# Performance work log

Hardware: AMD Instinct MI355X
Metric: run time of the kernel (lower is better)

Reference implementation:

```python
import jax, jax.numpy as jnp
import numpy as np

HEAD_DIM = 64
N_HEADS = 16
D_S = N_HEADS * HEAD_DIM  # 1024
D_Z = 128


def setup_inputs() -> dict:
    key = jax.random.key(0)
    ks = jax.random.split(key, 12)
    B, S = 1, 1024
    sc = 0.02
    return {
        "s": jax.random.normal(ks[0], (B, S, D_S), jnp.float32),
        "z": jax.random.normal(ks[1], (B, S, S, D_Z), jnp.float32),
        "wq": jax.random.normal(ks[2], (N_HEADS * HEAD_DIM, D_S), jnp.float32) * sc,
        "bq": jax.random.normal(ks[3], (N_HEADS * HEAD_DIM,), jnp.float32) * sc,
        "wk": jax.random.normal(ks[4], (N_HEADS * HEAD_DIM, D_S), jnp.float32) * sc,
        "wv": jax.random.normal(ks[5], (N_HEADS * HEAD_DIM, D_S), jnp.float32) * sc,
        "wg": jax.random.normal(ks[6], (N_HEADS * HEAD_DIM, D_S), jnp.float32) * sc,
        "z_norm_w": jnp.ones((D_Z,), jnp.float32),
        "z_norm_b": jnp.zeros((D_Z,), jnp.float32),
        "wz": jax.random.normal(ks[7], (N_HEADS, D_Z), jnp.float32) * sc,
        "wo": jax.random.normal(ks[8], (D_S, N_HEADS * HEAD_DIM), jnp.float32) * sc,
    }


def _layer_norm(x, w, b, eps=1e-5):
    mu = jnp.mean(x, axis=-1, keepdims=True)
    var = jnp.var(x, axis=-1, keepdims=True)
    return (x - mu) * jax.lax.rsqrt(var + eps) * w + b


def reference(s, z, wq, bq, wk, wv, wg, z_norm_w, z_norm_b, wz, wo):
    B, S, _ = s.shape
    H, hd = N_HEADS, HEAD_DIM
    # fused QKV projection (only q has bias in the original)
    q = (s @ wq.T + bq).reshape(B, S, H, hd)
    k = (s @ wk.T).reshape(B, S, H, hd)
    v = (s @ wv.T).reshape(B, S, H, hd)
    # pair bias: LN(z) -> linear D_Z -> H, permute to [B,H,S,S]
    zn = _layer_norm(z, z_norm_w, z_norm_b)
    bias = jnp.einsum("bijz,hz->bhij", zn, wz)  # [B,H,S,S]
    # attention with pair bias (net math: qk/sqrt(d) + bias)
    scores = jnp.einsum("bihd,bjhd->bhij", q, k) * (hd ** -0.5) + bias
    attn = jax.nn.softmax(scores, axis=-1)
    o = jnp.einsum("bhij,bjhd->bihd", attn, v).reshape(B, S, H * hd)
    # sigmoid gate then output projection
    g = jax.nn.sigmoid(s @ wg.T)
    return (o * g) @ wo.T
```

## Files before the change

### kernel.cpp

```cpp
#include <hip/hip_runtime.h>

typedef __attribute__((ext_vector_type(8))) short bf16x8;
typedef __attribute__((ext_vector_type(4))) float f32x4;

#define MFMA16(a,b,c) __builtin_amdgcn_mfma_f32_16x16x32_bf16(a,b,c,0,0,0)

__device__ __forceinline__ unsigned short f2bf(float f){
  unsigned int u = __float_as_uint(f);
  unsigned int r = (u + 0x7fffu + ((u >> 16) & 1u)) >> 16;
  return (unsigned short)r;
}
__device__ __forceinline__ float bf2f(unsigned short u){
  return __uint_as_float(((unsigned int)u) << 16);
}

__global__ __launch_bounds__(256) void prep_kernel(
    const float* __restrict__ s, const float* __restrict__ wq,
    const float* __restrict__ wk, const float* __restrict__ wv,
    const float* __restrict__ wg, const float* __restrict__ wo,
    unsigned short* __restrict__ sb, unsigned short* __restrict__ Wp,
    unsigned short* __restrict__ wob)
{
  const size_t M1 = 1u << 20;
  size_t base = ((size_t)blockIdx.x * 256 + threadIdx.x) * 4;
  const float* src; unsigned short* dst; size_t off;
  if (base < M1) { src = s; dst = sb; off = base; }
  else if (base < 5*M1) {
    size_t r = base - M1; int wsel = (int)(r >> 20);
    const float* wsrc0 = (wsel == 0) ? wq : (wsel == 1) ? wk : (wsel == 2) ? wv : wg;
    src = wsrc0; dst = Wp + ((size_t)wsel << 20); off = r & (M1 - 1);
  } else { src = wo; dst = wob; off = base - 5*M1; }
  float4 v = *(const float4*)(src + off);
  ushort4 o4;
  o4.x = f2bf(v.x); o4.y = f2bf(v.y); o4.z = f2bf(v.z); o4.w = f2bf(v.w);
  *(ushort4*)(dst + off) = o4;
}

__global__ __launch_bounds__(256) void wzprep_kernel(
    const float* __restrict__ wz, const float* __restrict__ znw,
    const float* __restrict__ znb, unsigned short* __restrict__ wzp,
    float* __restrict__ c12)
{
  __shared__ float r1[256], r2[256];
  int t = threadIdx.x; int h = t >> 4; int k0 = (t & 15) * 8;
  float p1 = 0.f, p2 = 0.f;
  for (int e = 0; e < 8; e++) {
    float wv = wz[h*128 + k0 + e];
    float w = znw[k0 + e], b = znb[k0 + e];
    wzp[h*128 + k0 + e] = f2bf(wv * w);
    p1 += wv * w; p2 += wv * b;
  }
  r1[t] = p1; r2[t] = p2;
  __syncthreads();
  if ((t & 15) == 0) {
    float s1 = 0.f, s2 = 0.f;
    for (int i = 0; i < 16; i++) { s1 += r1[t + i]; s2 += r2[t + i]; }
    c12[2*h] = s1; c12[2*h + 1] = s2;
  }
}

template<int MODE>
__global__ __launch_bounds__(256) void gemm_bf16(
    const unsigned short* __restrict__ A, const unsigned short* __restrict__ Bm,
    int M, int N, int K,
    const float* __restrict__ bq,
    unsigned short* __restrict__ qb, unsigned short* __restrict__ kb,
    unsigned short* __restrict__ vT, unsigned short* __restrict__ gb,
    float* __restrict__ outF)
{
  int lane = threadIdx.x & 63;
  int w = threadIdx.x >> 6;
  int lr = lane & 15, lg = lane >> 4;
  int row0 = blockIdx.y * 64 + (w & 1) * 32;
  int col0 = blockIdx.x * 128 + (w >> 1) * 64;
  f32x4 acc[2][4] = {};
  for (int kk = 0; kk < K; kk += 32) {
    bf16x8 af[2], bfr[4];
    #pragma unroll
    for (int t = 0; t < 2; t++)
      af[t] = *(const bf16x8*)(A + (size_t)(row0 + t*16 + lr) * K + kk + lg*8);
    #pragma unroll
    for (int t = 0; t < 4; t++)
      bfr[t] = *(const bf16x8*)(Bm + (size_t)(col0 + t*16 + lr) * K + kk + lg*8);
    #pragma unroll
    for (int a = 0; a < 2; a++)
      #pragma unroll
      for (int b = 0; b < 4; b++)
        acc[a][b] = MFMA16(af[a], bfr[b], acc[a][b]);
  }
  #pragma unroll
  for (int a = 0; a < 2; a++)
    #pragma unroll
    for (int b = 0; b < 4; b++)
      #pragma unroll
      for (int r = 0; r < 4; r++) {
        int m = row0 + a*16 + lg*4 + r;
        int n = col0 + b*16 + lr;
        float v = acc[a][b][r];
        if (MODE == 0) {
          if (n < 1024)      { v = (v + bq[n]) * 0.125f; qb[(size_t)m*1024 + n] = f2bf(v); }
          else if (n < 2048) { kb[(size_t)m*1024 + (n-1024)] = f2bf(v); }
          else if (n < 3072) { vT[(size_t)(n-2048)*1024 + m] = f2bf(v); }
          else               { float sg = 1.f / (1.f + __expf(-v)); gb[(size_t)m*1024 + (n-3072)] = f2bf(sg); }
        } else {
          outF[(size_t)m * N + n] = v;
        }
      }
}

__global__ __launch_bounds__(1024, 4) void fused_attn(
    const unsigned short* __restrict__ qb, const unsigned short* __restrict__ kb,
    const unsigned short* __restrict__ vT, const float* __restrict__ z,
    const unsigned short* __restrict__ wzp, const float* __restrict__ c12,
    float* __restrict__ op, float* __restrict__ ml, float* __restrict__ ll)
{
  __shared__ float biasT[16][16][68];
  __shared__ unsigned short P[16][1024];
  int w = threadIdx.x >> 6;
  int lane = threadIdx.x & 63;
  int jl = lane & 15, g = lane >> 4;
  int q0 = blockIdx.x * 16;
  int s = blockIdx.y;
  int h = w;
  unsigned short* Pw = P[w];

  bf16x8 af[4];
  #pragma unroll
  for (int mk = 0; mk < 4; mk++)
    af[mk] = *(const bf16x8*)(wzp + jl*128 + mk*32 + g*8);
  bf16x8 aq[2];
  #pragma unroll
  for (int kh = 0; kh < 2; kh++)
    aq[kh] = *(const bf16x8*)(qb + (size_t)(q0 + jl)*1024 + h*64 + kh*32 + g*8);
  float c1r[4], c2r[4];
  #pragma unroll
  for (int r = 0; r < 4; r++) {
    c1r[r] = c12[2*(g*4 + r)];
    c2r[r] = c12[2*(g*4 + r) + 1];
  }

  f32x4 od[4] = {};
  float m = -1e30f, ss = 0.f;

  for (int t = 0; t < 4; t++) {
    int jt = s*256 + t*64;

    #pragma unroll
    for (int it = 0; it < 4; it++) {
      int j = jt + it*16 + jl;
      const float* zp = z + ((size_t)(q0 + w)*1024 + j)*128;
      float4 zv[8];
      #pragma unroll
      for (int mk = 0; mk < 4; mk++) {
        zv[2*mk]   = *(const float4*)(zp + mk*32 + g*8);
        zv[2*mk+1] = *(const float4*)(zp + mk*32 + g*8 + 4);
      }
      float sum = 0.f, sq = 0.f;
      #pragma unroll
      for (int u = 0; u < 8; u++) {
        float4 v = zv[u];
        sum += v.x + v.y + v.z + v.w;
        sq = fmaf(v.x, v.x, fmaf(v.y, v.y, fmaf(v.z, v.z, fmaf(v.w, v.w, sq))));
      }
      sum += __shfl_xor(sum, 16); sum += __shfl_xor(sum, 32);
      sq  += __shfl_xor(sq, 16);  sq  += __shfl_xor(sq, 32);
      float mu = sum * (1.f/128.f);
      float rs = rsqrtf(sq * (1.f/128.f) - mu*mu + 1e-5f);
      f32x4 D = {0.f, 0.f, 0.f, 0.f};
      #pragma unroll
      for (int mk = 0; mk < 4; mk++) {
        float4 a = zv[2*mk], b = zv[2*mk+1];
        bf16x8 tf;
        tf[0] = (short)f2bf(a.x); tf[1] = (short)f2bf(a.y);
        tf[2] = (short)f2bf(a.z); tf[3] = (short)f2bf(a.w);
        tf[4] = (short)f2bf(b.x); tf[5] = (short)f2bf(b.y);
        tf[6] = (short)f2bf(b.z); tf[7] = (short)f2bf(b.w);
        D = MFMA16(af[mk], tf, D);
      }
      #pragma unroll
      for (int r = 0; r < 4; r++)
        biasT[g*4 + r][w][it*16 + jl] = rs*(D[r] - mu*c1r[r]) + c2r[r];
    }
    __syncthreads();

    f32x4 sc[4] = {};
    #pragma unroll
    for (int jb = 0; jb < 4; jb++)
      #pragma unroll
      for (int kh = 0; kh < 2; kh++) {
        bf16x8 bk = *(const bf16x8*)(kb + (size_t)(jt + jb*16 + jl)*1024 + h*64 + kh*32 + g*8);
        sc[jb] = MFMA16(bk, aq[kh], sc[jb]);
      }
    #pragma unroll
    for (int jb = 0; jb < 4; jb++) {
      f32x4 bl = *(const f32x4*)(&biasT[h][jl][jb*16 + g*4]);
      sc[jb][0] += bl[0]; sc[jb][1] += bl[1];
      sc[jb][2] += bl[2]; sc[jb][3] += bl[3];
    }

    float mx = -1e30f;
    #pragma unroll
    for (int jb = 0; jb < 4; jb++)
      #pragma unroll
      for (int r = 0; r < 4; r++) mx = fmaxf(mx, sc[jb][r]);
    mx = fmaxf(mx, __shfl_xor(mx, 16));
    mx = fmaxf(mx, __shfl_xor(mx, 32));
    float mn = fmaxf(m, mx);
    float a = __expf(m - mn);
    m = mn;
    float rsum = 0.f;
    #pragma unroll
    for (int jb = 0; jb < 4; jb++) {
      short4 pk;
      float p0 = __expf(sc[jb][0] - mn); rsum += p0; pk.x = (short)f2bf(p0);
      float p1 = __expf(sc[jb][1] - mn); rsum += p1; pk.y = (short)f2bf(p1);
      float p2 = __expf(sc[jb][2] - mn); rsum += p2; pk.z = (short)f2bf(p2);
      float p3 = __expf(sc[jb][3] - mn); rsum += p3; pk.w = (short)f2bf(p3);
      int b = jb*2 + (g >> 1);
      int bpz = b ^ (jl & 7);
      *(short4*)(Pw + jl*64 + bpz*8 + (g & 1)*4) = pk;
    }
    ss = ss * a + rsum;

    float albc[4];
    #pragma unroll
    for (int r = 0; r < 4; r++) albc[r] = __shfl(a, g*4 + r);
    #pragma unroll
    for (int db = 0; db < 4; db++)
      #pragma unroll
      for (int r = 0; r < 4; r++) od[db][r] *= albc[r];

    #pragma unroll
    for (int jh = 0; jh < 2; jh++) {
      int b = jh*4 + g;
      int bpz = b ^ (jl & 7);
      bf16x8 ap = *(const bf16x8*)(Pw + jl*64 + bpz*8);
      #pragma unroll
      for (int db = 0; db < 4; db++) {
        bf16x8 bv = *(const bf16x8*)(vT + (size_t)(h*64 + db*16 + jl)*1024 + jt + jh*32 + g*8);
        od[db] = MFMA16(ap, bv, od[db]);
      }
    }
    __syncthreads();
  }

  ss += __shfl_xor(ss, 16);
  ss += __shfl_xor(ss, 32);

  size_t base = ((size_t)(s*16 + h) * 1024);
  #pragma unroll
  for (int db = 0; db < 4; db++)
    #pragma unroll
    for (int r = 0; r < 4; r++) {
      int q = q0 + g*4 + r;
      op[(base + q)*64 + db*16 + jl] = od[db][r];
    }
  if (g == 0) {
    ml[base + q0 + jl] = m;
    ll[base + q0 + jl] = ss;
  }
}

__global__ __launch_bounds__(256) void combine_kernel(
    const float* __restrict__ op, const float* __restrict__ ml,
    const float* __restrict__ ll, const unsigned short* __restrict__ gb,
    unsigned short* __restrict__ og)
{
  int t = blockIdx.x * 256 + threadIdx.x;
  int d4 = t & 15;
  int q = (t >> 4) & 1023;
  int h = t >> 14;

  float mv[4], lv[4];
  float mstar = -1e30f;
  #pragma unroll
  for (int s = 0; s < 4; s++) {
    mv[s] = ml[(size_t)(s*16 + h)*1024 + q];
    lv[s] = ll[(size_t)(s*16 + h)*1024 + q];
    mstar = fmaxf(mstar, mv[s]);
  }
  float lsum = 0.f;
  float ws[4];
  #pragma unroll
  for (int s = 0; s < 4; s++) {
    ws[s] = __expf(mv[s] - mstar);
    lsum = fmaf(ws[s], lv[s], lsum);
  }
  float inv = 1.f / lsum;

  float4 o = {0.f, 0.f, 0.f, 0.f};
  #pragma unroll
  for (int s = 0; s < 4; s++) {
    float4 p = *(const float4*)(op + ((size_t)(s*16 + h)*1024 + q)*64 + d4*4);
    o.x = fmaf(ws[s], p.x, o.x); o.y = fmaf(ws[s], p.y, o.y);
    o.z = fmaf(ws[s], p.z, o.z); o.w = fmaf(ws[s], p.w, o.w);
  }
  ushort4 gv = *(const ushort4*)(gb + (size_t)q*1024 + h*64 + d4*4);
  ushort4 r;
  r.x = f2bf(o.x * inv * bf2f(gv.x));
  r.y = f2bf(o.y * inv * bf2f(gv.y));
  r.z = f2bf(o.z * inv * bf2f(gv.z));
  r.w = f2bf(o.w * inv * bf2f(gv.w));
  *(ushort4*)(og + (size_t)q*1024 + h*64 + d4*4) = r;
}

extern "C" void kernel_launch(void* const* d_in, const int* in_sizes, int n_in,
                              void* d_out, int out_size, void* d_ws, size_t ws_size,
                              hipStream_t stream) {
  const float* s   = (const float*)d_in[0];
  const float* z   = (const float*)d_in[1];
  const float* wq  = (const float*)d_in[2];
  const float* bq  = (const float*)d_in[3];
  const float* wk  = (const float*)d_in[4];
  const float* wv  = (const float*)d_in[5];
  const float* wg  = (const float*)d_in[6];
  const float* znw = (const float*)d_in[7];
  const float* znb = (const float*)d_in[8];
  const float* wz  = (const float*)d_in[9];
  const float* wo  = (const float*)d_in[10];
  float* out = (float*)d_out;

  char* ws = (char*)d_ws;
  unsigned short* qbuf  = (unsigned short*)(ws + ((size_t)64 << 20));
  unsigned short* kbuf  = (unsigned short*)(ws + ((size_t)66 << 20));
  unsigned short* vTb   = (unsigned short*)(ws + ((size_t)68 << 20));
  unsigned short* gbuf  = (unsigned short*)(ws + ((size_t)70 << 20));
  unsigned short* ogb   = (unsigned short*)(ws + ((size_t)72 << 20));
  unsigned short* sb    = (unsigned short*)(ws + ((size_t)74 << 20));
  unsigned short* Wp    = (unsigned short*)(ws + ((size_t)76 << 20));
  unsigned short* wob   = (unsigned short*)(ws + ((size_t)84 << 20));
  unsigned short* wzp   = (unsigned short*)(ws + ((size_t)86 << 20));
  float*          c12   = (float*)(ws + ((size_t)86 << 20) + 4096);
  float*          opart = (float*)(ws + ((size_t)96 << 20));
  float*          mlb   = (float*)(ws + ((size_t)112 << 20));
  float*          llb   = (float*)(ws + ((size_t)113 << 20));

  prep_kernel<<<6144, 256, 0, stream>>>(s, wq, wk, wv, wg, wo, sb, Wp, wob);
  wzprep_kernel<<<1, 256, 0, stream>>>(wz, znw, znb, wzp, c12);
  gemm_bf16<0><<<dim3(32, 16), 256, 0, stream>>>(sb, Wp, 1024, 4096, 1024, bq,
                                                 qbuf, kbuf, vTb, gbuf, nullptr);
  fused_attn<<<dim3(64, 4), 1024, 0, stream>>>(qbuf, kbuf, vTb, z, wzp, c12,
                                               opart, mlb, llb);
  combine_kernel<<<1024, 256, 0, stream>>>(opart, mlb, llb, gbuf, ogb);
  gemm_bf16<1><<<dim3(8, 16), 256, 0, stream>>>(ogb, wob, 1024, 1024, 1024, nullptr,
                                                nullptr, nullptr, nullptr, nullptr, out);
}
```

Measured before the change: 234.7 us.

## Merge wz prep into prep kernel, pad bias LDS, shrink z-tile register footprint

Folds the single-block wz/LN-weight preparation into an extra block of the prep kernel, removing one kernel launch. In the fused attention kernel, the bias shared array gets a padded middle dimension to reduce LDS bank conflicts. The z-loading loop now converts each float4 pair to bf16 immediately instead of keeping all eight float4s live, and the outer loops are no longer unrolled, to cut register pressure. Disabling unrolling may reduce memory-level parallelism in the z streaming loop.

```diff
diff --git a/kernel.cpp b/kernel.cpp
--- a/kernel.cpp
+++ b/kernel.cpp
@@ -18,9 +18,31 @@
     const float* __restrict__ s, const float* __restrict__ wq,
     const float* __restrict__ wk, const float* __restrict__ wv,
     const float* __restrict__ wg, const float* __restrict__ wo,
+    const float* __restrict__ wz, const float* __restrict__ znw,
+    const float* __restrict__ znb,
     unsigned short* __restrict__ sb, unsigned short* __restrict__ Wp,
-    unsigned short* __restrict__ wob)
+    unsigned short* __restrict__ wob,
+    unsigned short* __restrict__ wzp, float* __restrict__ c12)
 {
+  __shared__ float r1[256], r2[256];
+  if (blockIdx.x == 6144) {
+    int t = threadIdx.x; int h = t >> 4; int k0 = (t & 15) * 8;
+    float p1 = 0.f, p2 = 0.f;
+    for (int e = 0; e < 8; e++) {
+      float wvv = wz[h*128 + k0 + e];
+      float w = znw[k0 + e], b = znb[k0 + e];
+      wzp[h*128 + k0 + e] = f2bf(wvv * w);
+      p1 += wvv * w; p2 += wvv * b;
+    }
+    r1[t] = p1; r2[t] = p2;
+    __syncthreads();
+    if ((t & 15) == 0) {
+      float s1 = 0.f, s2 = 0.f;
+      for (int i = 0; i < 16; i++) { s1 += r1[t + i]; s2 += r2[t + i]; }
+      c12[2*h] = s1; c12[2*h + 1] = s2;
+    }
+    return;
+  }
   const size_t M1 = 1u << 20;
   size_t base = ((size_t)blockIdx.x * 256 + threadIdx.x) * 4;
   const float* src; unsigned short* dst; size_t off;
@@ -34,29 +56,6 @@
   ushort4 o4;
   o4.x = f2bf(v.x); o4.y = f2bf(v.y); o4.z = f2bf(v.z); o4.w = f2bf(v.w);
   *(ushort4*)(dst + off) = o4;
-}
-
-__global__ __launch_bounds__(256) void wzprep_kernel(
-    const float* __restrict__ wz, const float* __restrict__ znw,
-    const float* __restrict__ znb, unsigned short* __restrict__ wzp,
-    float* __restrict__ c12)
-{
-  __shared__ float r1[256], r2[256];
-  int t = threadIdx.x; int h = t >> 4; int k0 = (t & 15) * 8;
-  float p1 = 0.f, p2 = 0.f;
-  for (int e = 0; e < 8; e++) {
-    float wv = wz[h*128 + k0 + e];
-    float w = znw[k0 + e], b = znb[k0 + e];
-    wzp[h*128 + k0 + e] = f2bf(wv * w);
-    p1 += wv * w; p2 += wv * b;
-  }
-  r1[t] = p1; r2[t] = p2;
-  __syncthreads();
-  if ((t & 15) == 0) {
-    float s1 = 0.f, s2 = 0.f;
-    for (int i = 0; i < 16; i++) { s1 += r1[t + i]; s2 += r2[t + i]; }
-    c12[2*h] = s1; c12[2*h + 1] = s2;
-  }
 }
 
 template<int MODE>
@@ -114,7 +113,7 @@
     const unsigned short* __restrict__ wzp, const float* __restrict__ c12,
     float* __restrict__ op, float* __restrict__ ml, float* __restrict__ ll)
 {
-  __shared__ float biasT[16][16][68];
+  __shared__ float biasT[16][17][68];
   __shared__ unsigned short P[16][1024];
   int w = threadIdx.x >> 6;
   int lane = threadIdx.x & 63;
@@ -142,25 +141,29 @@
   f32x4 od[4] = {};
   float m = -1e30f, ss = 0.f;
 
+  #pragma unroll 1
   for (int t = 0; t < 4; t++) {
     int jt = s*256 + t*64;
 
-    #pragma unroll
+    #pragma unroll 1
     for (int it = 0; it < 4; it++) {
       int j = jt + it*16 + jl;
       const float* zp = z + ((size_t)(q0 + w)*1024 + j)*128;
-      float4 zv[8];
+      bf16x8 tf[4];
+      float sum = 0.f, sq = 0.f;
       #pragma unroll
       for (int mk = 0; mk < 4; mk++) {
-        zv[2*mk]   = *(const float4*)(zp + mk*32 + g*8);
-        zv[2*mk+1] = *(const float4*)(zp + mk*32 + g*8 + 4);
-      }
-      float sum = 0.f, sq = 0.f;
-      #pragma unroll
-      for (int u = 0; u < 8; u++) {
-        float4 v = zv[u];
-        sum += v.x + v.y + v.z + v.w;
-        sq = fmaf(v.x, v.x, fmaf(v.y, v.y, fmaf(v.z, v.z, fmaf(v.w, v.w, sq))));
+        float4 a = *(const float4*)(zp + mk*32 + g*8);
+        float4 b = *(const float4*)(zp + mk*32 + g*8 + 4);
+        sum += a.x + a.y + a.z + a.w + b.x + b.y + b.z + b.w;
+        sq = fmaf(a.x, a.x, fmaf(a.y, a.y, fmaf(a.z, a.z, fmaf(a.w, a.w, sq))));
+        sq = fmaf(b.x, b.x, fmaf(b.y, b.y, fmaf(b.z, b.z, fmaf(b.w, b.w, sq))));
+        bf16x8 tv;
+        tv[0] = (short)f2bf(a.x); tv[1] = (short)f2bf(a.y);
+        tv[2] = (short)f2bf(a.z); tv[3] = (short)f2bf(a.w);
+        tv[4] = (short)f2bf(b.x); tv[5] = (short)f2bf(b.y);
+        tv[6] = (short)f2bf(b.z); tv[7] = (short)f2bf(b.w);
+        tf[mk] = tv;
       }
       sum += __shfl_xor(sum, 16); sum += __shfl_xor(sum, 32);
       sq  += __shfl_xor(sq, 16);  sq  += __shfl_xor(sq, 32);
@@ -168,15 +171,8 @@
       float rs = rsqrtf(sq * (1.f/128.f) - mu*mu + 1e-5f);
       f32x4 D = {0.f, 0.f, 0.f, 0.f};
       #pragma unroll
-      for (int mk = 0; mk < 4; mk++) {
-        float4 a = zv[2*mk], b = zv[2*mk+1];
-        bf16x8 tf;
-        tf[0] = (short)f2bf(a.x); tf[1] = (short)f2bf(a.y);
-        tf[2] = (short)f2bf(a.z); tf[3] = (short)f2bf(a.w);
-        tf[4] = (short)f2bf(b.x); tf[5] = (short)f2bf(b.y);
-        tf[6] = (short)f2bf(b.z); tf[7] = (short)f2bf(b.w);
-        D = MFMA16(af[mk], tf, D);
-      }
+      for (int mk = 0; mk < 4; mk++)
+        D = MFMA16(af[mk], tf[mk], D);
       #pragma unroll
       for (int r = 0; r < 4; r++)
         biasT[g*4 + r][w][it*16 + jl] = rs*(D[r] - mu*c1r[r]) + c2r[r];
@@ -335,8 +331,8 @@
   float*          mlb   = (float*)(ws + ((size_t)112 << 20));
   float*          llb   = (float*)(ws + ((size_t)113 << 20));
 
-  prep_kernel<<<6144, 256, 0, stream>>>(s, wq, wk, wv, wg, wo, sb, Wp, wob);
-  wzprep_kernel<<<1, 256, 0, stream>>>(wz, znw, znb, wzp, c12);
+  prep_kernel<<<6145, 256, 0, stream>>>(s, wq, wk, wv, wg, wo, wz, znw, znb,
+                                        sb, Wp, wob, wzp, c12);
   gemm_bf16<0><<<dim3(32, 16), 256, 0, stream>>>(sb, Wp, 1024, 4096, 1024, bq,
                                                  qbuf, kbuf, vTb, gbuf, nullptr);
   fused_attn<<<dim3(64, 4), 1024, 0, stream>>>(qbuf, kbuf, vTb, z, wzp, c12,
```

Measured after the change: 229.1 us. -2.4%, faster.
